# Kernel tuning notes

Hardware: AMD Instinct MI355X
Metric: run time of the kernel (lower is better)

## Reference

```python
import jax, jax.numpy as jnp
import numpy as np

BETA = 0.1


def setup_inputs() -> dict:
    key = jax.random.key(0)
    ks = jax.random.split(key, 8)
    B, S, H, V = 4, 512, 2048, 32000
    return {
        "lin_weight": jax.random.normal(ks[0], (V, H), jnp.float32) * 0.02,
        "_input": jax.random.normal(ks[1], (B, S, H), jnp.float32),
        "attention_mask": jnp.ones((B, S), jnp.float32),
        "rewards": jax.random.normal(ks[2], (B,), jnp.float32),
        "bias": jax.random.normal(ks[3], (V,), jnp.float32) * 0.02,
        "ref_input": jax.random.normal(ks[4], (B, S, H), jnp.float32),
        "ref_weight": jax.random.normal(ks[5], (V, H), jnp.float32) * 0.02,
        "ref_bias": jax.random.normal(ks[6], (V,), jnp.float32) * 0.02,
    }


def _seq_logps(x, w, b, mask):
    # logits: [B,S,V]; per-token max log-softmax, masked, summed over seq
    logits = jnp.einsum("bsh,vh->bsv", x, w) + b
    lp = jax.nn.log_softmax(logits, axis=-1)
    seq = (jnp.max(lp, axis=-1) * mask).sum(axis=-1)  # [B]
    return logits, seq


def reference(lin_weight, _input, attention_mask, rewards, bias, ref_input, ref_weight, ref_bias):
    policy_logits, seq_log_probs = _seq_logps(_input, lin_weight, bias, attention_mask)
    _, ref_seq_logps = _seq_logps(ref_input, ref_weight, ref_bias, attention_mask)
    ref_seq_logps = jax.lax.stop_gradient(ref_seq_logps)

    adv = rewards - rewards.mean()
    std = jnp.std(rewards, ddof=1)  # torch unbiased std
    adv = jnp.where(std > 0, adv / std, adv)

    kl_div = seq_log_probs - ref_seq_logps
    loss = (-(adv * seq_log_probs) + BETA * kl_div).mean()

    metrics = (
        seq_log_probs.mean(),
        jnp.std(seq_log_probs, ddof=1),
        policy_logits.mean(),
        kl_div.mean(),
    )
    return (loss,) + metrics
```

## Files before the change

### kernel.cpp

```cpp
#include <hip/hip_runtime.h>
#include <hip/hip_fp16.h>
#include <math.h>

#define TOK 2048
#define HD 2048
#define VOC 32000
#define BM 256
#define BN 256
#define BK 64
#define NT (HD/BK)
#define NCH (VOC/64)
#define NBLK ((TOK/BM)*(VOC/BN))

typedef _Float16 half8 __attribute__((ext_vector_type(8)));
typedef float float4v __attribute__((ext_vector_type(4)));

#define GLB __attribute__((address_space(1)))
#define LDSAS __attribute__((address_space(3)))

static __device__ __forceinline__ void gload_lds16(const void* g, void* l) {
  __builtin_amdgcn_global_load_lds((const GLB unsigned int*)g,
                                   (LDSAS unsigned int*)l, 16, 0, 0);
}

__global__ void cvt_f32_f16(const float* __restrict__ in,
                            _Float16* __restrict__ out, int n8) {
  for (int i = blockIdx.x * blockDim.x + threadIdx.x; i < n8;
       i += gridDim.x * blockDim.x) {
    float4v a = *(const float4v*)(in + (size_t)i*8);
    float4v b = *(const float4v*)(in + (size_t)i*8 + 4);
    half8 h;
    #pragma unroll
    for (int j=0;j<4;j++) { h[j] = (_Float16)a[j]; h[4+j] = (_Float16)b[j]; }
    *(half8*)(out + (size_t)i*8) = h;
  }
}

template<int CB, bool SG1, bool SG2, int VMN>
__device__ __forceinline__ void ktile(
    unsigned char* ldsby, const char* Xb, const char* Wb,
    int sA0, int sA1, int sB0, int sB1, int ldst0, int ldst1, int kbn,
    const int (&aofs)[2][8], const int (&bofs)[2][4], float4v (&acc)[8][4])
{
  constexpr int BI = CB ? 1 : 0;
  half8 af[8], bf[4];

  #pragma unroll
  for (int n=0;n<4;n++) bf[n] = *(const half8*)(ldsby + bofs[BI][n] + 16384);
  #pragma unroll
  for (int m=0;m<8;m++) af[m] = *(const half8*)(ldsby + aofs[BI][m]);
  if (SG1) {
    gload_lds16(Xb + (sA0 + kbn + 64), ldsby + ((CB^65536) + 32768) + ldst0);
    gload_lds16(Xb + (sA1 + kbn + 64), ldsby + ((CB^65536) + 32768) + ldst1);
    gload_lds16(Wb + (sB0 + kbn + 64), ldsby + ((CB^65536) + 49152) + ldst0);
    gload_lds16(Wb + (sB1 + kbn + 64), ldsby + ((CB^65536) + 49152) + ldst1);
  }
  asm volatile("s_waitcnt lgkmcnt(4)" ::: "memory");
  __builtin_amdgcn_sched_barrier(0);
  __builtin_amdgcn_s_setprio(1);
  #pragma unroll
  for (int m=0;m<4;m++)
    #pragma unroll
    for (int n=0;n<4;n++)
      acc[m][n] = __builtin_amdgcn_mfma_f32_16x16x32_f16(af[m], bf[n], acc[m][n],0,0,0);
  asm volatile("s_waitcnt lgkmcnt(0)" ::: "memory");
  __builtin_amdgcn_sched_barrier(0);
  #pragma unroll
  for (int m=4;m<8;m++)
    #pragma unroll
    for (int n=0;n<4;n++)
      acc[m][n] = __builtin_amdgcn_mfma_f32_16x16x32_f16(af[m], bf[n], acc[m][n],0,0,0);
  __builtin_amdgcn_s_setprio(0);
  __builtin_amdgcn_s_barrier();

  #pragma unroll
  for (int n=0;n<4;n++) bf[n] = *(const half8*)(ldsby + bofs[BI][n] + 49152);
  #pragma unroll
  for (int m=0;m<8;m++) af[m] = *(const half8*)(ldsby + aofs[BI][m] + 32768);
  if (SG2) {
    gload_lds16(Xb + (sA0 + kbn + 128), ldsby + (CB + 0)     + ldst0);
    gload_lds16(Xb + (sA1 + kbn + 128), ldsby + (CB + 0)     + ldst1);
    gload_lds16(Wb + (sB0 + kbn + 128), ldsby + (CB + 16384) + ldst0);
    gload_lds16(Wb + (sB1 + kbn + 128), ldsby + (CB + 16384) + ldst1);
  }
  asm volatile("s_waitcnt lgkmcnt(4)" ::: "memory");
  __builtin_amdgcn_sched_barrier(0);
  __builtin_amdgcn_s_setprio(1);
  #pragma unroll
  for (int m=0;m<4;m++)
    #pragma unroll
    for (int n=0;n<4;n++)
      acc[m][n] = __builtin_amdgcn_mfma_f32_16x16x32_f16(af[m], bf[n], acc[m][n],0,0,0);
  asm volatile("s_waitcnt lgkmcnt(0)" ::: "memory");
  __builtin_amdgcn_sched_barrier(0);
  #pragma unroll
  for (int m=4;m<8;m++)
    #pragma unroll
    for (int n=0;n<4;n++)
      acc[m][n] = __builtin_amdgcn_mfma_f32_16x16x32_f16(af[m], bf[n], acc[m][n],0,0,0);
  __builtin_amdgcn_s_setprio(0);
  if (VMN == 4)      asm volatile("s_waitcnt vmcnt(4)" ::: "memory");
  else if (VMN == 0) asm volatile("s_waitcnt vmcnt(0)" ::: "memory");
  __builtin_amdgcn_s_barrier();
}

__global__ __launch_bounds__(512, 2) void gemm_stats_f16(
    const _Float16* __restrict__ Xh, const _Float16* __restrict__ Wh,
    const float* __restrict__ bias,
    float* __restrict__ pmax, float* __restrict__ psum,
    float* __restrict__ bsum, int computeSum)
{
  __shared__ unsigned char ldsbuf[131072];
  unsigned char* ldsby = ldsbuf;

  int bid = blockIdx.x;
  int swz = (bid & 7) * (NBLK/8) + (bid >> 3);
  int rowt = swz & 7;
  int colt = swz >> 3;
  int brow = rowt * BM;
  int bcol = colt * BN;

  int tid  = threadIdx.x;
  int lane = tid & 63;
  int wv   = tid >> 6;
  int wr   = wv >> 2;
  int wc   = wv & 3;
  int l15  = lane & 15;
  int q    = lane >> 4;

  int aofs[2][8], bofs[2][4];
  #pragma unroll
  for (int m = 0; m < 8; m++) {
    int r = wr*128 + m*16 + l15;
    int o = r*64 + (((q + r + (r>>2)) & 3) << 4);
    aofs[0][m] = o; aofs[1][m] = o + 65536;
  }
  #pragma unroll
  for (int n = 0; n < 4; n++) {
    int r = wc*64 + n*16 + l15;
    int o = r*64 + (((q + r + (r>>2)) & 3) << 4);
    bofs[0][n] = o; bofs[1][n] = o + 65536;
  }

  int r0 = tid >> 2, c0 = tid & 3;
  int r1 = r0 + 128;
  int q0 = (c0 - r0 - (r0>>2)) & 3;
  int q1 = (c0 - r1 - (r1>>2)) & 3;
  int sA0 = (brow + r0)*(HD*2) + (q0<<4);
  int sA1 = (brow + r1)*(HD*2) + (q1<<4);
  int sB0 = (bcol + r0)*(HD*2) + (q0<<4);
  int sB1 = (bcol + r1)*(HD*2) + (q1<<4);
  int ldst0 = (wv<<10);
  int ldst1 = (wv<<10) + 8192;

  const char* Xb = (const char*)Xh;
  const char* Wb = (const char*)Wh;

  float4v acc[8][4];
  #pragma unroll
  for (int m=0;m<8;m++)
    #pragma unroll
    for (int n=0;n<4;n++) acc[m][n] = (float4v){0.f,0.f,0.f,0.f};

  gload_lds16(Xb + sA0,       ldsby + 0     + ldst0);
  gload_lds16(Xb + sA1,       ldsby + 0     + ldst1);
  gload_lds16(Wb + sB0,       ldsby + 16384 + ldst0);
  gload_lds16(Wb + sB1,       ldsby + 16384 + ldst1);
  gload_lds16(Xb + (sA0+64),  ldsby + 32768 + ldst0);
  gload_lds16(Xb + (sA1+64),  ldsby + 32768 + ldst1);
  gload_lds16(Wb + (sB0+64),  ldsby + 49152 + ldst0);
  gload_lds16(Wb + (sB1+64),  ldsby + 49152 + ldst1);
  gload_lds16(Xb + (sA0+128), ldsby + 65536 + ldst0);
  gload_lds16(Xb + (sA1+128), ldsby + 65536 + ldst1);
  gload_lds16(Wb + (sB0+128), ldsby + 81920 + ldst0);
  gload_lds16(Wb + (sB1+128), ldsby + 81920 + ldst1);
  asm volatile("s_waitcnt vmcnt(4)" ::: "memory");
  __builtin_amdgcn_s_barrier();

  int kbn = 128;
  #pragma unroll 1
  for (int i = 0; i < 15; ++i) {
    ktile<0,     true, true, 4>(ldsby, Xb, Wb, sA0,sA1,sB0,sB1, ldst0,ldst1, kbn, aofs, bofs, acc);
    kbn += 128;
    ktile<65536, true, true, 4>(ldsby, Xb, Wb, sA0,sA1,sB0,sB1, ldst0,ldst1, kbn, aofs, bofs, acc);
    kbn += 128;
  }
  ktile<0,     true,  false, 0>(ldsby, Xb, Wb, sA0,sA1,sB0,sB1, ldst0,ldst1, kbn, aofs, bofs, acc);
  kbn += 128;
  ktile<65536, false, false, -1>(ldsby, Xb, Wb, sA0,sA1,sB0,sB1, ldst0,ldst1, kbn, aofs, bofs, acc);

  float bv[4];
  #pragma unroll
  for (int n=0;n<4;n++) bv[n] = bias[bcol + wc*64 + n*16 + l15];

  float lsum = 0.f;
  int ch = colt*4 + wc;
  #pragma unroll
  for (int m=0;m<8;m++) {
    #pragma unroll
    for (int r=0;r<4;r++) {
      float v0 = acc[m][0][r] + bv[0];
      float v1 = acc[m][1][r] + bv[1];
      float v2 = acc[m][2][r] + bv[2];
      float v3 = acc[m][3][r] + bv[3];
      if (computeSum) lsum += v0+v1+v2+v3;
      float mx = fmaxf(fmaxf(v0,v1), fmaxf(v2,v3));
      #pragma unroll
      for (int off=1; off<16; off<<=1) mx = fmaxf(mx, __shfl_xor(mx, off, 64));
      float se = __expf(v0-mx)+__expf(v1-mx)+__expf(v2-mx)+__expf(v3-mx);
      #pragma unroll
      for (int off=1; off<16; off<<=1) se += __shfl_xor(se, off, 64);
      if (l15 == 0) {
        int row = brow + wr*128 + m*16 + (lane>>4)*4 + r;
        pmax[(size_t)row*NCH + ch] = mx;
        psum[(size_t)row*NCH + ch] = se;
      }
    }
  }

  if (computeSum) {
    #pragma unroll
    for (int off=1; off<64; off<<=1) lsum += __shfl_xor(lsum, off, 64);
    __syncthreads();
    float* red = (float*)ldsbuf;
    if (lane == 0) red[wv] = lsum;
    __syncthreads();
    if (tid == 0) {
      float s = 0.f;
      for (int w=0; w<8; w++) s += red[w];
      bsum[blockIdx.x] = s;
    }
  }
}

__global__ void row_combine(const float* __restrict__ pmax,
                            const float* __restrict__ psum,
                            const float* __restrict__ mask,
                            float* __restrict__ tok)
{
  int row = blockIdx.x;
  int lane = threadIdx.x;
  float M = -INFINITY;
  for (int c = lane; c < NCH; c += 64) M = fmaxf(M, pmax[(size_t)row*NCH + c]);
  #pragma unroll
  for (int off=1; off<64; off<<=1) M = fmaxf(M, __shfl_xor(M, off, 64));
  float L = 0.f;
  for (int c = lane; c < NCH; c += 64)
    L += psum[(size_t)row*NCH + c] * __expf(pmax[(size_t)row*NCH + c] - M);
  #pragma unroll
  for (int off=1; off<64; off<<=1) L += __shfl_xor(L, off, 64);
  if (lane == 0) tok[row] = -logf(L) * mask[row];
}

__global__ void finalize(const float* __restrict__ tokP,
                         const float* __restrict__ tokR,
                         const float* __restrict__ rewards,
                         const float* __restrict__ bsum, int nbsum,
                         float* __restrict__ out)
{
  __shared__ float red[256];
  __shared__ float seqP[4], seqR[4];
  int t = threadIdx.x;
  for (int b=0; b<4; b++) {
    float v = tokP[b*512 + t] + tokP[b*512 + 256 + t];
    red[t] = v; __syncthreads();
    for (int s=128; s>0; s>>=1) { if (t < s) red[t] += red[t+s]; __syncthreads(); }
    if (t == 0) seqP[b] = red[0];
    __syncthreads();
    v = tokR[b*512 + t] + tokR[b*512 + 256 + t];
    red[t] = v; __syncthreads();
    for (int s=128; s>0; s>>=1) { if (t < s) red[t] += red[t+s]; __syncthreads(); }
    if (t == 0) seqR[b] = red[0];
    __syncthreads();
  }
  float ls = 0.f;
  for (int i=t; i<nbsum; i+=256) ls += bsum[i];
  red[t] = ls; __syncthreads();
  for (int s=128; s>0; s>>=1) { if (t < s) red[t] += red[t+s]; __syncthreads(); }
  if (t == 0) {
    float r0=rewards[0], r1=rewards[1], r2=rewards[2], r3=rewards[3];
    float rm = (r0+r1+r2+r3)*0.25f;
    float var = ((r0-rm)*(r0-rm)+(r1-rm)*(r1-rm)+(r2-rm)*(r2-rm)+(r3-rm)*(r3-rm))/3.f;
    float rstd = sqrtf(var);
    float adv[4] = {r0-rm, r1-rm, r2-rm, r3-rm};
    if (rstd > 0.f) { for (int b=0;b<4;b++) adv[b] /= rstd; }
    float loss=0.f, sm=0.f, km=0.f;
    for (int b=0;b<4;b++) {
      float kl = seqP[b] - seqR[b];
      loss += -(adv[b]*seqP[b]) + 0.1f*kl;
      sm += seqP[b]; km += kl;
    }
    loss *= 0.25f; sm *= 0.25f; km *= 0.25f;
    float sv = 0.f;
    for (int b=0;b<4;b++) { float d = seqP[b]-sm; sv += d*d; }
    float sstd = sqrtf(sv/3.f);
    out[0] = loss;
    out[1] = sm;
    out[2] = sstd;
    out[3] = red[0] / ((float)TOK * (float)VOC);
    out[4] = km;
  }
}

extern "C" void kernel_launch(void* const* d_in, const int* in_sizes, int n_in,
                              void* d_out, int out_size, void* d_ws, size_t ws_size,
                              hipStream_t stream) {
  const float* W    = (const float*)d_in[0];
  const float* X    = (const float*)d_in[1];
  const float* mask = (const float*)d_in[2];
  const float* rew  = (const float*)d_in[3];
  const float* bias = (const float*)d_in[4];
  const float* Xr   = (const float*)d_in[5];
  const float* Wr   = (const float*)d_in[6];
  const float* br   = (const float*)d_in[7];
  float* out = (float*)d_out;

  float* pmax = (float*)d_ws;
  float* psum = pmax + (size_t)TOK*NCH;
  float* tokP = psum + (size_t)TOK*NCH;
  float* tokR = tokP + TOK;
  float* bsum = tokR + TOK;

  size_t headFloats = (size_t)TOK*NCH*2 + TOK*2 + 4096;
  size_t offXh = headFloats * 4;
  _Float16* Xh = (_Float16*)((unsigned char*)d_ws + offXh);
  _Float16* Wh = (_Float16*)((unsigned char*)d_ws + offXh + (size_t)TOK*HD*2);

  cvt_f32_f16<<<2048, 256, 0, stream>>>(X,  Xh, TOK*HD/8);
  cvt_f32_f16<<<2048, 256, 0, stream>>>(W,  Wh, VOC*HD/8);
  gemm_stats_f16<<<NBLK, 512, 0, stream>>>(Xh, Wh, bias, pmax, psum, bsum, 1);
  row_combine<<<TOK, 64, 0, stream>>>(pmax, psum, mask, tokP);
  cvt_f32_f16<<<2048, 256, 0, stream>>>(Xr, Xh, TOK*HD/8);
  cvt_f32_f16<<<2048, 256, 0, stream>>>(Wr, Wh, VOC*HD/8);
  gemm_stats_f16<<<NBLK, 512, 0, stream>>>(Xh, Wh, br, pmax, psum, bsum, 0);
  row_combine<<<TOK, 64, 0, stream>>>(pmax, psum, mask, tokR);
  finalize<<<1, 256, 0, stream>>>(tokP, tokR, rew, bsum, NBLK, out);
}
```

Baseline: 706.2 us.

## Use XOR-swizzled LDS layout and prefetch next-half fragments during MFMAs

Replaces the LDS swizzle with an XOR-based layout over 8 sub-columns that pairs two rows per 128-byte line, rewriting both the global-to-LDS store mapping and the fragment read offsets. It also removes the explicit lgkmcnt waits and sched barriers, and issues the second half-tile's fragment loads in the middle of the first half's MFMAs, splitting the A fragments into lo and hi groups so LDS reads overlap matrix math. The goal is fewer LDS bank conflicts and better hiding of LDS latency. It relies on the compiler to insert correct waits, and register pressure increases because more fragments are live at once.

New measurement: 678.5 us. 1.04x faster.

```diff
diff --git a/kernel.cpp b/kernel.cpp
--- a/kernel.cpp
+++ b/kernel.cpp
@@ -23,6 +23,10 @@
                                    (LDSAS unsigned int*)l, 16, 0, 0);
 }
 
+static __device__ __forceinline__ float4v mfma16(half8 a, half8 b, float4v c) {
+  return __builtin_amdgcn_mfma_f32_16x16x32_f16(a, b, c, 0, 0, 0);
+}
+
 __global__ void cvt_f32_f16(const float* __restrict__ in,
                             _Float16* __restrict__ out, int n8) {
   for (int i = blockIdx.x * blockDim.x + threadIdx.x; i < n8;
@@ -40,64 +44,58 @@
 __device__ __forceinline__ void ktile(
     unsigned char* ldsby, const char* Xb, const char* Wb,
     int sA0, int sA1, int sB0, int sB1, int ldst0, int ldst1, int kbn,
-    const int (&aofs)[2][8], const int (&bofs)[2][4], float4v (&acc)[8][4])
+    const int (&aofs)[8], const int (&bofs)[4], float4v (&acc)[8][4])
 {
-  constexpr int BI = CB ? 1 : 0;
-  half8 af[8], bf[4];
-
-  #pragma unroll
-  for (int n=0;n<4;n++) bf[n] = *(const half8*)(ldsby + bofs[BI][n] + 16384);
-  #pragma unroll
-  for (int m=0;m<8;m++) af[m] = *(const half8*)(ldsby + aofs[BI][m]);
+  constexpr int U0 = CB, U1 = CB + 16384, U2 = CB + 32768, U3 = CB + 49152;
+  half8 af1[8], bf1[4], af2lo[4], bf2[4], af2hi[4];
+
+  #pragma unroll
+  for (int n=0;n<4;n++) bf1[n] = *(const half8*)(ldsby + U1 + bofs[n]);
+  #pragma unroll
+  for (int m=0;m<8;m++) af1[m] = *(const half8*)(ldsby + U0 + aofs[m]);
   if (SG1) {
     gload_lds16(Xb + (sA0 + kbn + 64), ldsby + ((CB^65536) + 32768) + ldst0);
     gload_lds16(Xb + (sA1 + kbn + 64), ldsby + ((CB^65536) + 32768) + ldst1);
     gload_lds16(Wb + (sB0 + kbn + 64), ldsby + ((CB^65536) + 49152) + ldst0);
     gload_lds16(Wb + (sB1 + kbn + 64), ldsby + ((CB^65536) + 49152) + ldst1);
   }
-  asm volatile("s_waitcnt lgkmcnt(4)" ::: "memory");
-  __builtin_amdgcn_sched_barrier(0);
   __builtin_amdgcn_s_setprio(1);
   #pragma unroll
   for (int m=0;m<4;m++)
     #pragma unroll
     for (int n=0;n<4;n++)
-      acc[m][n] = __builtin_amdgcn_mfma_f32_16x16x32_f16(af[m], bf[n], acc[m][n],0,0,0);
-  asm volatile("s_waitcnt lgkmcnt(0)" ::: "memory");
-  __builtin_amdgcn_sched_barrier(0);
+      acc[m][n] = mfma16(af1[m], bf1[n], acc[m][n]);
+  #pragma unroll
+  for (int n=0;n<4;n++) bf2[n]   = *(const half8*)(ldsby + U3 + bofs[n]);
+  #pragma unroll
+  for (int m=0;m<4;m++) af2lo[m] = *(const half8*)(ldsby + U2 + aofs[m]);
   #pragma unroll
   for (int m=4;m<8;m++)
     #pragma unroll
     for (int n=0;n<4;n++)
-      acc[m][n] = __builtin_amdgcn_mfma_f32_16x16x32_f16(af[m], bf[n], acc[m][n],0,0,0);
+      acc[m][n] = mfma16(af1[m], bf1[n], acc[m][n]);
   __builtin_amdgcn_s_setprio(0);
   __builtin_amdgcn_s_barrier();
 
   #pragma unroll
-  for (int n=0;n<4;n++) bf[n] = *(const half8*)(ldsby + bofs[BI][n] + 49152);
-  #pragma unroll
-  for (int m=0;m<8;m++) af[m] = *(const half8*)(ldsby + aofs[BI][m] + 32768);
+  for (int m=0;m<4;m++) af2hi[m] = *(const half8*)(ldsby + U2 + aofs[4+m]);
   if (SG2) {
     gload_lds16(Xb + (sA0 + kbn + 128), ldsby + (CB + 0)     + ldst0);
     gload_lds16(Xb + (sA1 + kbn + 128), ldsby + (CB + 0)     + ldst1);
     gload_lds16(Wb + (sB0 + kbn + 128), ldsby + (CB + 16384) + ldst0);
     gload_lds16(Wb + (sB1 + kbn + 128), ldsby + (CB + 16384) + ldst1);
   }
-  asm volatile("s_waitcnt lgkmcnt(4)" ::: "memory");
-  __builtin_amdgcn_sched_barrier(0);
   __builtin_amdgcn_s_setprio(1);
   #pragma unroll
   for (int m=0;m<4;m++)
     #pragma unroll
     for (int n=0;n<4;n++)
-      acc[m][n] = __builtin_amdgcn_mfma_f32_16x16x32_f16(af[m], bf[n], acc[m][n],0,0,0);
-  asm volatile("s_waitcnt lgkmcnt(0)" ::: "memory");
-  __builtin_amdgcn_sched_barrier(0);
-  #pragma unroll
-  for (int m=4;m<8;m++)
+      acc[m][n] = mfma16(af2lo[m], bf2[n], acc[m][n]);
+  #pragma unroll
+  for (int m=0;m<4;m++)
     #pragma unroll
     for (int n=0;n<4;n++)
-      acc[m][n] = __builtin_amdgcn_mfma_f32_16x16x32_f16(af[m], bf[n], acc[m][n],0,0,0);
+      acc[4+m][n] = mfma16(af2hi[m], bf2[n], acc[4+m][n]);
   __builtin_amdgcn_s_setprio(0);
   if (VMN == 4)      asm volatile("s_waitcnt vmcnt(4)" ::: "memory");
   else if (VMN == 0) asm volatile("s_waitcnt vmcnt(0)" ::: "memory");
@@ -128,30 +126,22 @@
   int l15  = lane & 15;
   int q    = lane >> 4;
 
-  int aofs[2][8], bofs[2][4];
-  #pragma unroll
-  for (int m = 0; m < 8; m++) {
-    int r = wr*128 + m*16 + l15;
-    int o = r*64 + (((q + r + (r>>2)) & 3) << 4);
-    aofs[0][m] = o; aofs[1][m] = o + 65536;
-  }
-  #pragma unroll
-  for (int n = 0; n < 4; n++) {
-    int r = wc*64 + n*16 + l15;
-    int o = r*64 + (((q + r + (r>>2)) & 3) << 4);
-    bofs[0][n] = o; bofs[1][n] = o + 65536;
-  }
-
-  int r0 = tid >> 2, c0 = tid & 3;
-  int r1 = r0 + 128;
-  int q0 = (c0 - r0 - (r0>>2)) & 3;
-  int q1 = (c0 - r1 - (r1>>2)) & 3;
-  int sA0 = (brow + r0)*(HD*2) + (q0<<4);
-  int sA1 = (brow + r1)*(HD*2) + (q1<<4);
-  int sB0 = (bcol + r0)*(HD*2) + (q0<<4);
-  int sB1 = (bcol + r1)*(HD*2) + (q1<<4);
-  int ldst0 = (wv<<10);
-  int ldst1 = (wv<<10) + 8192;
+  int aswz = (((((l15 & 1) << 2) | q) ^ ((l15 >> 1) & 7)) << 4) + ((l15 >> 1) << 7);
+  int aofs[8], bofs[4];
+  #pragma unroll
+  for (int m = 0; m < 8; m++) aofs[m] = wr*8192 + m*1024 + aswz;
+  #pragma unroll
+  for (int n = 0; n < 4; n++) bofs[n] = wc*4096 + n*1024 + aswz;
+
+  int s8  = (tid & 7) ^ ((tid >> 3) & 7);
+  int rl  = wv*16 + (((tid >> 3) & 7) << 1) + (s8 >> 2);
+  int kc  = (s8 & 3) << 4;
+  int sA0 = (brow + rl)*(HD*2) + kc;
+  int sA1 = sA0 + 128*(HD*2);
+  int sB0 = (bcol + rl)*(HD*2) + kc;
+  int sB1 = sB0 + 128*(HD*2);
+  int ldst0 = (wv << 10);
+  int ldst1 = (wv << 10) + 8192;
 
   const char* Xb = (const char*)Xh;
   const char* Wb = (const char*)Wh;
```
